# Optimization experiments

Measured on AMD Instinct MI355X. Metric: run time of the kernel, lower is better.

## Reference

```python
import jax, jax.numpy as jnp
import numpy as np

BN_EPS = 1e-5
TEMPERATURE = 256 ** 0.5  # sqrt(c2), since cv3 = ScaledDotProductAttention(c2)


def conv_bn_silu(x, w, gamma, beta, mean, var):
    # Conv2d(k=3, s=1, pad='same', bias=False) -> BatchNorm2d (running stats) -> SiLU
    y = jax.lax.conv_general_dilated(
        x, w, window_strides=(1, 1), padding='SAME',
        dimension_numbers=('NCHW', 'OIHW', 'NCHW'))
    scale = (gamma / jnp.sqrt(var + BN_EPS))[None, :, None, None]
    shift = (beta - mean * gamma / jnp.sqrt(var + BN_EPS))[None, :, None, None]
    y = y * scale + shift
    return y * jax.nn.sigmoid(y)  # SiLU


def setup_inputs() -> dict:
    key = jax.random.key(0)
    ks = jax.random.split(key, 8)
    B, C, H, W = 16, 256, 64, 64
    Ch = 128  # hidden channels c_ = int(c2 * e)
    x = jax.random.normal(ks[0], (B, C, H, W), dtype=jnp.float32)
    w1 = jax.random.normal(ks[1], (Ch, C, 3, 3), dtype=jnp.float32) * 0.05
    g1 = jnp.ones((Ch,), jnp.float32) + 0.1 * jax.random.normal(ks[2], (Ch,), dtype=jnp.float32)
    b1 = 0.1 * jax.random.normal(ks[3], (Ch,), dtype=jnp.float32)
    m1 = 0.1 * jax.random.normal(ks[4], (Ch,), dtype=jnp.float32)
    v1 = jnp.ones((Ch,), jnp.float32) + 0.5 * jax.random.uniform(ks[5], (Ch,), dtype=jnp.float32)
    w2 = jax.random.normal(ks[6], (C, Ch, 3, 3), dtype=jnp.float32) * 0.05
    g2 = jnp.ones((C,), jnp.float32)
    b2 = jnp.zeros((C,), jnp.float32)
    m2 = 0.1 * jax.random.normal(ks[7], (C,), dtype=jnp.float32)
    v2 = jnp.ones((C,), jnp.float32) + 0.5 * jax.random.uniform(jax.random.fold_in(key, 99), (C,), dtype=jnp.float32)
    return {"x": x, "w1": w1, "g1": g1, "b1": b1, "m1": m1, "v1": v1,
            "w2": w2, "g2": g2, "b2": b2, "m2": m2, "v2": v2}


def reference(x, w1, g1, b1, m1, v1, w2, g2, b2, m2, v2):
    y = conv_bn_silu(x, w1, g1, b1, m1, v1)       # [B, 128, H, W]
    y = conv_bn_silu(y, w2, g2, b2, m2, v2)       # [B, 256, H, W]
    B, C, H, W = y.shape
    q = y.reshape(B, C, H * W)                    # q = k^T = v, all views of y
    # channel-channel attention: scores [B, C, C]
    scores = jnp.einsum('bcn,bdn->bcd', q / TEMPERATURE, q)
    attn = jax.nn.softmax(scores, axis=-1)        # dropout is identity in eval
    out = jnp.einsum('bcd,bdn->bcn', attn, q).reshape(B, C, H, W)
    return x + out  # shortcut: c1 == c2
```

## Files before the change

### kernel.cpp

```cpp
#include <hip/hip_runtime.h>
#include <math.h>

#define BB 16
#define C1 256
#define CHD 128
#define NN 4096
#define INV_T (1.0f/16.0f)

typedef _Float16 half8 __attribute__((ext_vector_type(8)));
typedef __attribute__((ext_vector_type(4))) float f32x4;
typedef __attribute__((ext_vector_type(16))) float f32x16;

__device__ inline unsigned short f2h(float f) {
    _Float16 h = (_Float16)f;
    return __builtin_bit_cast(unsigned short, h);
}

#define GLDS(g, l) __builtin_amdgcn_global_load_lds(                              \
    (const __attribute__((address_space(1))) unsigned int*)(g),                   \
    (__attribute__((address_space(3))) unsigned int*)(l), 16, 0, 0)

__device__ inline void xcd_remap(int& bx, int& by, int& bz) {
    int gx = gridDim.x, gy = gridDim.y;
    int lin = blockIdx.x + gx * (blockIdx.y + gy * blockIdx.z);
    int cpx = (gx * gy * (int)gridDim.z) >> 3;
    lin = (lin & 7) * cpx + (lin >> 3);
    bx = lin % gx; int t = lin / gx; by = t % gy; bz = t / gy;
}

__global__ __launch_bounds__(256) void nchw_to_nhwc_f16(
    const float* __restrict__ x, unsigned short* __restrict__ xh, int C)
{
    const int c0 = blockIdx.x * 64;
    const int hp = blockIdx.y;
    const int b  = blockIdx.z;
    const int nCk = C >> 4;

    if (hp == 0 || hp == 65) {
        for (int idx = threadIdx.x; idx < 1024; idx += 256) {
            int w = idx >> 4, cq = (idx & 15) * 4;
            ushort4 z; z.x = z.y = z.z = z.w = 0;
            *(ushort4*)&xh[((((size_t)b * nCk + (c0 >> 4) + (cq >> 4)) * 66 + hp) * 64 + w) * 16
                           + (cq & 15)] = z;
        }
        return;
    }
    const int h = hp - 1;
    __shared__ float ts[64][65];
    for (int idx = threadIdx.x; idx < 4096; idx += 256) {
        int cl = idx >> 6, w = idx & 63;
        ts[cl][w] = x[(((size_t)b * C + c0 + cl) * 64 + h) * 64 + w];
    }
    __syncthreads();
    for (int idx = threadIdx.x; idx < 1024; idx += 256) {
        int w = idx >> 4, cq = (idx & 15) * 4;
        ushort4 o;
        o.x = f2h(ts[cq + 0][w]); o.y = f2h(ts[cq + 1][w]);
        o.z = f2h(ts[cq + 2][w]); o.w = f2h(ts[cq + 3][w]);
        *(ushort4*)&xh[((((size_t)b * nCk + (c0 >> 4) + (cq >> 4)) * 66 + hp) * 64 + w) * 16
                       + (cq & 15)] = o;
    }
}

__global__ __launch_bounds__(256) void pack_w_kernel(
    const float* __restrict__ w, unsigned short* __restrict__ wT, int Cout, int Cin)
{
    int idx = blockIdx.x * 256 + threadIdx.x;
    int total = Cout * Cin * 9;
    if (idx >= total) return;
    int ci = idx % Cin; int t = idx / Cin; int co = t % Cout; int kk = t / Cout;
    wT[((((size_t)(ci >> 4)) * 9 + kk) * Cout + co) * 16 + (ci & 15)] =
        f2h(w[((size_t)co * Cin + ci) * 9 + kk]);
}

__global__ __launch_bounds__(256) void zero_y1h_pads(unsigned short* __restrict__ y1h)
{
    int idx = blockIdx.x * 256 + threadIdx.x;
    int b   = idx >> 12;
    int ck  = (idx >> 9) & 7;
    int row = ((idx >> 8) & 1) ? 65 : 0;
    int w   = (idx >> 2) & 63;
    int qtr = idx & 3;
    ushort4 z; z.x = z.y = z.z = z.w = 0;
    *(ushort4*)&y1h[((((size_t)b * 8 + ck) * 66 + row) * 64 + w) * 16 + qtr * 4] = z;
}

__global__ __launch_bounds__(512, 4) void conv_mfma_kernel(
    const unsigned short* __restrict__ xh, const unsigned short* __restrict__ wT,
    const float* __restrict__ gamma, const float* __restrict__ beta,
    const float* __restrict__ mean, const float* __restrict__ var,
    unsigned short* __restrict__ outNHWC,
    unsigned short* __restrict__ yhi, unsigned short* __restrict__ yhiT,
    int Cin, int Cout)
{
    int bx, by, bz;
    xcd_remap(bx, by, bz);
    const int tid  = threadIdx.x;
    const int wid  = tid >> 6;
    const int lane = tid & 63;
    const int l31  = lane & 31;
    const int hi   = lane >> 5;
    const int coBase = bx * 64;
    const int h0     = by * 8;
    const int b      = bz;
    const int nCk    = Cin >> 4;

    __shared__ __align__(16) unsigned short smem[39552];
    __shared__ float bnsc[64], bnsh[64];

    if (tid < 64) {
        int co = coBase + tid;
        float sc = gamma[co] * rsqrtf(var[co] + 1e-5f);
        bnsc[tid] = sc;
        bnsh[tid] = beta[co] - mean[co] * sc;
    }
    if (tid < 160) {
        int cell = tid >> 2;
        int part = tid & 3;
        int buf  = cell & 1;
        int col  = ((cell >> 1) & 1) ? 65 : 0;
        int r    = cell >> 2;
        ushort4 z; z.x = z.y = z.z = z.w = 0;
        *(ushort4*)&smem[buf * 10560 + (r * 66 + col) * 16 + part * 4] = z;
    }

    auto stage = [&](int sel, int ck) {
        unsigned short* wsd = smem + 21120 + sel * 9216;
        unsigned short* xsd = smem + sel * 10560;
        for (int it = wid; it < 38; it += 8) {
            if (it < 18) {
                int kk = it >> 1, h = it & 1;
                const unsigned short* g =
                    wT + (((size_t)ck * 9 + kk) * Cout + coBase + h * 32) * 16 + lane * 8;
                GLDS(g, wsd + (kk * 64 + h * 32) * 16);
            } else {
                int j = it - 18;
                int r = j >> 1, hf = j & 1;
                const unsigned short* g =
                    xh + ((((size_t)b * nCk + ck) * 66 + h0 + r) * 64 + hf * 32) * 16 + lane * 8;
                GLDS(g, xsd + (r * 66 + 1 + hf * 32) * 16);
            }
        }
    };

    stage(0, 0);
    __syncthreads();

    f32x16 acc[2][2] = {};

    int sel = 0;
    for (int ck = 0; ck < nCk; ck++) {
        if (ck + 1 < nCk) stage(sel ^ 1, ck + 1);

        const unsigned short* wsb = smem + 21120 + sel * 9216;
        const unsigned short* xsb = smem + sel * 10560;
        __builtin_amdgcn_s_setprio(1);
#pragma unroll
        for (int kk = 0; kk < 9; kk++) {
            const int kh = kk / 3, kw = kk % 3;
            half8 a0 = *(const half8*)&wsb[(kk * 64 +      l31) * 16 + hi * 8];
            half8 a1 = *(const half8*)&wsb[(kk * 64 + 32 + l31) * 16 + hi * 8];
            const unsigned short* xr = &xsb[((wid + kh) * 66 + l31 + kw) * 16 + hi * 8];
            half8 b0 = *(const half8*)xr;
            half8 b1 = *(const half8*)&xr[32 * 16];
            acc[0][0] = __builtin_amdgcn_mfma_f32_32x32x16_f16(a0, b0, acc[0][0], 0, 0, 0);
            acc[0][1] = __builtin_amdgcn_mfma_f32_32x32x16_f16(a0, b1, acc[0][1], 0, 0, 0);
            acc[1][0] = __builtin_amdgcn_mfma_f32_32x32x16_f16(a1, b0, acc[1][0], 0, 0, 0);
            acc[1][1] = __builtin_amdgcn_mfma_f32_32x32x16_f16(a1, b1, acc[1][1], 0, 0, 0);
        }
        __builtin_amdgcn_s_setprio(0);
        __syncthreads();
        sel ^= 1;
    }

    const int orow = h0 + wid;
    const bool isConv1 = (outNHWC != nullptr);

    __syncthreads();

#pragma unroll
    for (int mi = 0; mi < 2; mi++)
#pragma unroll
        for (int ni = 0; ni < 2; ni++) {
            f32x16 a = acc[mi][ni];
            int w = ni * 32 + l31;
            int swz = ((l31 + wid) & 7) << 3;
#pragma unroll
            for (int rq = 0; rq < 4; rq++) {
                int c0 = mi * 32 + rq * 8 + hi * 4;
                ushort4 o; unsigned short* op = (unsigned short*)&o;
#pragma unroll
                for (int r = 0; r < 4; r++) {
                    float t = a[rq * 4 + r] * bnsc[c0 + r] + bnsh[c0 + r];
                    float s = t / (1.f + __expf(-t));
                    op[r] = f2h(s);
                    if (!isConv1)
                        yhi[(((size_t)b * Cout + coBase + c0 + r) * 64 + orow) * 64 + w] = op[r];
                }
                *(ushort4*)&smem[wid * 4096 + w * 64 + (c0 ^ swz)] = o;
            }
        }
    __syncthreads();

    const int ckB = bx * 4;
    const int nCkOut = Cout >> 4;
#pragma unroll
    for (int j = 0; j < 8; j++) {
        int g   = j * 512 + tid;
        int s   = g & 1;
        int w   = (g >> 1) & 63;
        int row = (g >> 7) & 7;
        int ck  = g >> 10;
        uint4 v = *(const uint4*)&smem[row * 4096 + w * 64 +
                     (((ck * 2 + s) * 8) ^ (((w + row) & 7) << 3))];
        if (isConv1) {
            *(uint4*)&outNHWC[((((size_t)b * nCkOut + ckB + ck) * 66 + h0 + row + 1) * 64 + w) * 16
                              + s * 8] = v;
        } else {
            *(uint4*)&yhiT[(((size_t)b * nCkOut + ckB + ck) * 4096 + (size_t)(h0 + row) * 64 + w) * 16
                           + s * 8] = v;
        }
    }
}

__global__ __launch_bounds__(256) void scores_mfma_kernel(
    const unsigned short* __restrict__ yhi, float* __restrict__ scores)
{
    static const int TI[10] = {0,0,0,0,1,1,1,2,2,3};
    static const int TJ[10] = {0,1,2,3,1,2,3,2,3,3};
    int bx, by, bz;
    xcd_remap(bx, by, bz);
    const int b  = bz;
    const int kh = by;
    const int ti = TI[bx], tj = TJ[bx];
    const int cB = ti * 64;
    const int dB = tj * 64;
    const int tid  = threadIdx.x;
    const int wid  = tid >> 6;
    const int lane = tid & 63;
    const int ln   = lane & 15;
    const int q    = lane >> 4;
    const int wm   = wid >> 1, wn = wid & 1;

    float* scp = scores + (size_t)kh * 1048576;

    __shared__ unsigned short As[64 * 128];
    __shared__ unsigned short Bs[64 * 128];

    const int rl = lane >> 4;
    const int gl = lane & 15;

    f32x4 acc[2][2] = {};

    for (int ck = kh * 16; ck < kh * 16 + 16; ck++) {
        const int n0 = ck * 128;
        for (int it = wid; it < 32; it += 4) {
            const int tile = it >> 4;
            const int j = it & 15;
            const int r = j * 4 + rl;
            const int gq = gl ^ (r & 7);
            const int rowAbs = (tile ? dB : cB) + r;
            const unsigned short* g =
                yhi + ((size_t)b * 256 + rowAbs) * 4096 + n0 + gq * 8;
            GLDS(g, (tile ? Bs : As) + j * 512);
        }
        __syncthreads();

#pragma unroll
        for (int kwin = 0; kwin < 4; kwin++) {
            half8 ah[2], bh[2];
#pragma unroll
            for (int mi = 0; mi < 2; mi++) {
                int row = wm * 32 + mi * 16 + ln;
                ah[mi] = *(const half8*)&As[row * 128 + ((kwin * 4 + q) ^ (ln & 7)) * 8];
            }
#pragma unroll
            for (int ni = 0; ni < 2; ni++) {
                int row = wn * 32 + ni * 16 + ln;
                bh[ni] = *(const half8*)&Bs[row * 128 + ((kwin * 4 + q) ^ (ln & 7)) * 8];
            }
#pragma unroll
            for (int mi = 0; mi < 2; mi++)
#pragma unroll
                for (int ni = 0; ni < 2; ni++)
                    acc[mi][ni] = __builtin_amdgcn_mfma_f32_16x16x32_f16(
                        ah[mi], bh[ni], acc[mi][ni], 0, 0, 0);
        }
        __syncthreads();
    }

#pragma unroll
    for (int mi = 0; mi < 2; mi++)
#pragma unroll
        for (int ni = 0; ni < 2; ni++) {
            f32x4 a = acc[mi][ni];
            float vals[4];
            vals[0] = a.x * INV_T; vals[1] = a.y * INV_T;
            vals[2] = a.z * INV_T; vals[3] = a.w * INV_T;
            int c0 = cB + wm * 32 + mi * 16 + q * 4;
            int d  = dB + wn * 32 + ni * 16 + ln;
#pragma unroll
            for (int r = 0; r < 4; r++)
                scp[((size_t)b * C1 + c0 + r) * C1 + d] = vals[r];
            if (ti != tj) {
                float4 tv = {vals[0], vals[1], vals[2], vals[3]};
                *(float4*)&scp[((size_t)b * C1 + d) * C1 + c0] = tv;
            }
        }
}

__global__ __launch_bounds__(64) void softmax_kernel(
    const float* __restrict__ scores, unsigned short* __restrict__ attn16)
{
    const int row = blockIdx.x;
    const float* p = scores + (size_t)row * C1;
    const int lane = threadIdx.x;

    float4 v0 = ((const float4*)p)[lane];
    float4 v1 = ((const float4*)(p + 1048576))[lane];
    float4 v;
    v.x = v0.x + v1.x; v.y = v0.y + v1.y;
    v.z = v0.z + v1.z; v.w = v0.w + v1.w;
    float m = fmaxf(fmaxf(v.x, v.y), fmaxf(v.z, v.w));
#pragma unroll
    for (int off = 32; off >= 1; off >>= 1)
        m = fmaxf(m, __shfl_xor(m, off, 64));

    float4 e;
    e.x = expf(v.x - m); e.y = expf(v.y - m);
    e.z = expf(v.z - m); e.w = expf(v.w - m);
    float s = e.x + e.y + e.z + e.w;
#pragma unroll
    for (int off = 32; off >= 1; off >>= 1)
        s += __shfl_xor(s, off, 64);
    float inv = 1.f / s;
    ushort4 o;
    o.x = f2h(e.x * inv); o.y = f2h(e.y * inv);
    o.z = f2h(e.z * inv); o.w = f2h(e.w * inv);
    *(ushort4*)&attn16[(size_t)row * C1 + lane * 4] = o;
}

__global__ __launch_bounds__(256) void out_mfma_kernel(
    const unsigned short* __restrict__ attn16, const unsigned short* __restrict__ yhiT,
    const float* __restrict__ x, float* __restrict__ out)
{
    int bx, by, bz;
    xcd_remap(bx, by, bz);
    const int b  = bz;
    const int cB = by * 64;
    const int nB = bx * 128;
    const int tid  = threadIdx.x;
    const int wid  = tid >> 6;
    const int lane = tid & 63;
    const int ln   = lane & 15;
    const int q    = lane >> 4;
    const int wm   = wid >> 1, wn = wid & 1;

    __shared__ unsigned short As[64 * 64];
    __shared__ unsigned short Bs[4 * 128 * 16];

    const int r8 = lane >> 3;
    const int gq = (lane & 7) ^ r8;

    f32x4 acc[2][4] = {};

    for (int ck = 0; ck < 4; ck++) {
        const int d0 = ck * 64;
        for (int it = wid; it < 24; it += 4) {
            if (it < 8) {
                const unsigned short* g =
                    attn16 + ((size_t)b * 256 + cB + it * 8 + r8) * 256 + d0 + gq * 8;
                GLDS(g, As + it * 512);
            } else {
                int j = it - 8;
                int u = j >> 2, part = j & 3;
                const unsigned short* g =
                    yhiT + (((size_t)b * 16 + ck * 4 + u) * 4096 + nB + part * 32) * 16 + lane * 8;
                GLDS(g, Bs + (u * 128 + part * 32) * 16);
            }
        }
        __syncthreads();

#pragma unroll
        for (int kwin = 0; kwin < 2; kwin++) {
            const int cc = (((kwin * 4 + q) ^ (ln & 7))) * 8;
            const int gK = kwin * 4 + q;
            half8 af[2], bfr[4];
#pragma unroll
            for (int mi = 0; mi < 2; mi++)
                af[mi] = *(const half8*)&As[(wm * 32 + mi * 16 + ln) * 64 + cc];
#pragma unroll
            for (int ni = 0; ni < 4; ni++) {
                int row = wn * 64 + ni * 16 + ln;
                bfr[ni] = *(const half8*)&Bs[(gK >> 1) * 2048 + row * 16 + (gK & 1) * 8];
            }
#pragma unroll
            for (int mi = 0; mi < 2; mi++)
#pragma unroll
                for (int ni = 0; ni < 4; ni++)
                    acc[mi][ni] = __builtin_amdgcn_mfma_f32_16x16x32_f16(
                        af[mi], bfr[ni], acc[mi][ni], 0, 0, 0);
        }
        __syncthreads();
    }

#pragma unroll
    for (int mi = 0; mi < 2; mi++)
#pragma unroll
        for (int ni = 0; ni < 4; ni++) {
            f32x4 a = acc[mi][ni];
            float vals[4] = {a.x, a.y, a.z, a.w};
#pragma unroll
            for (int r = 0; r < 4; r++) {
                int c = cB + wm * 32 + mi * 16 + q * 4 + r;
                int n = nB + wn * 64 + ni * 16 + ln;
                size_t o = ((size_t)b * C1 + c) * NN + n;
                out[o] = x[o] + vals[r];
            }
        }
}

extern "C" void kernel_launch(void* const* d_in, const int* in_sizes, int n_in,
                              void* d_out, int out_size, void* d_ws, size_t ws_size,
                              hipStream_t stream)
{
    const float* x  = (const float*)d_in[0];
    const float* w1 = (const float*)d_in[1];
    const float* g1 = (const float*)d_in[2];
    const float* b1 = (const float*)d_in[3];
    const float* m1 = (const float*)d_in[4];
    const float* v1 = (const float*)d_in[5];
    const float* w2 = (const float*)d_in[6];
    const float* g2 = (const float*)d_in[7];
    const float* b2 = (const float*)d_in[8];
    const float* m2 = (const float*)d_in[9];
    const float* v2 = (const float*)d_in[10];
    float* out = (float*)d_out;

    unsigned short* xh   = (unsigned short*)d_ws;
    unsigned short* y1h  = xh  + (size_t)17301504;
    unsigned short* wt1  = y1h + (size_t)8650752;
    unsigned short* wt2  = wt1 + (size_t)294912;
    unsigned short* yhiT = wt2 + (size_t)294912;
    unsigned short* yhi  = xh;
    float*          sc   = (float*)y1h;
    unsigned short* attn16 = (unsigned short*)(sc + 2097152);

    nchw_to_nhwc_f16<<<dim3(C1 / 64, 66, BB), 256, 0, stream>>>(x, xh, C1);
    pack_w_kernel<<<(9 * CHD * C1 + 255) / 256, 256, 0, stream>>>(w1, wt1, CHD, C1);
    pack_w_kernel<<<(9 * C1 * CHD + 255) / 256, 256, 0, stream>>>(w2, wt2, C1, CHD);
    zero_y1h_pads<<<256, 256, 0, stream>>>(y1h);

    conv_mfma_kernel<<<dim3(CHD / 64, 8, BB), 512, 0, stream>>>(
        xh, wt1, g1, b1, m1, v1, y1h, nullptr, nullptr, C1, CHD);
    conv_mfma_kernel<<<dim3(C1 / 64, 8, BB), 512, 0, stream>>>(
        y1h, wt2, g2, b2, m2, v2, nullptr, yhi, yhiT, CHD, C1);

    scores_mfma_kernel<<<dim3(10, 2, BB), 256, 0, stream>>>(yhi, sc);
    softmax_kernel<<<dim3(BB * C1), 64, 0, stream>>>(sc, attn16);
    out_mfma_kernel<<<dim3(NN / 128, 4, BB), 256, 0, stream>>>(attn16, yhiT, x, out);
}
```

Baseline: 299.8 us.

## Split 16-channel chunks into two 8-channel halves for conv LDS layout

Changes the packed fp16 layout of inputs, weights and the conv1 intermediate from [..][w][16 channels] to [..][half][w][8 channels], so each MFMA operand read in the conv kernel hits contiguous 16-byte rows per half-wave. The goal is to remove LDS bank conflicts caused by the 32-byte stride between lanes in the old interleaved layout. Producers, padding zeroing, staging and the conv1 output store are all updated to match. The risk is a layout mismatch between producers and consumers, or different conflict patterns at the padded column offsets.

```diff
diff --git a/kernel.cpp b/kernel.cpp
--- a/kernel.cpp
+++ b/kernel.cpp
@@ -39,9 +39,10 @@
     if (hp == 0 || hp == 65) {
         for (int idx = threadIdx.x; idx < 1024; idx += 256) {
             int w = idx >> 4, cq = (idx & 15) * 4;
+            int ck = (c0 >> 4) + (cq >> 4), half = (cq >> 3) & 1, rem = cq & 7;
             ushort4 z; z.x = z.y = z.z = z.w = 0;
-            *(ushort4*)&xh[((((size_t)b * nCk + (c0 >> 4) + (cq >> 4)) * 66 + hp) * 64 + w) * 16
-                           + (cq & 15)] = z;
+            *(ushort4*)&xh[(((((size_t)b * nCk + ck) * 66 + hp) * 2 + half) * 64 + w) * 8
+                           + rem] = z;
         }
         return;
     }
@@ -54,11 +55,12 @@
     __syncthreads();
     for (int idx = threadIdx.x; idx < 1024; idx += 256) {
         int w = idx >> 4, cq = (idx & 15) * 4;
+        int ck = (c0 >> 4) + (cq >> 4), half = (cq >> 3) & 1, rem = cq & 7;
         ushort4 o;
         o.x = f2h(ts[cq + 0][w]); o.y = f2h(ts[cq + 1][w]);
         o.z = f2h(ts[cq + 2][w]); o.w = f2h(ts[cq + 3][w]);
-        *(ushort4*)&xh[((((size_t)b * nCk + (c0 >> 4) + (cq >> 4)) * 66 + hp) * 64 + w) * 16
-                       + (cq & 15)] = o;
+        *(ushort4*)&xh[(((((size_t)b * nCk + ck) * 66 + hp) * 2 + half) * 64 + w) * 8
+                       + rem] = o;
     }
 }
 
@@ -69,7 +71,8 @@
     int total = Cout * Cin * 9;
     if (idx >= total) return;
     int ci = idx % Cin; int t = idx / Cin; int co = t % Cout; int kk = t / Cout;
-    wT[((((size_t)(ci >> 4)) * 9 + kk) * Cout + co) * 16 + (ci & 15)] =
+    int ck = ci >> 4, half = (ci >> 3) & 1, rem = ci & 7;
+    wT[((((size_t)ck * 9 + kk) * 2 + half) * Cout + co) * 8 + rem] =
         f2h(w[((size_t)co * Cin + ci) * 9 + kk]);
 }
 
@@ -79,10 +82,9 @@
     int b   = idx >> 12;
     int ck  = (idx >> 9) & 7;
     int row = ((idx >> 8) & 1) ? 65 : 0;
-    int w   = (idx >> 2) & 63;
-    int qtr = idx & 3;
+    int inner = (idx & 255) * 4;
     ushort4 z; z.x = z.y = z.z = z.w = 0;
-    *(ushort4*)&y1h[((((size_t)b * 8 + ck) * 66 + row) * 64 + w) * 16 + qtr * 4] = z;
+    *(ushort4*)&y1h[(((size_t)b * 8 + ck) * 66 + row) * 1024 + inner] = z;
 }
 
 __global__ __launch_bounds__(512, 4) void conv_mfma_kernel(
@@ -114,14 +116,14 @@
         bnsc[tid] = sc;
         bnsh[tid] = beta[co] - mean[co] * sc;
     }
-    if (tid < 160) {
-        int cell = tid >> 2;
-        int part = tid & 3;
-        int buf  = cell & 1;
-        int col  = ((cell >> 1) & 1) ? 65 : 0;
-        int r    = cell >> 2;
+    if (tid < 80) {
+        int buf  = tid & 1;
+        int col  = ((tid >> 1) & 1) ? 65 : 0;
+        int half = (tid >> 2) & 1;
+        int r    = tid >> 3;
         ushort4 z; z.x = z.y = z.z = z.w = 0;
-        *(ushort4*)&smem[buf * 10560 + (r * 66 + col) * 16 + part * 4] = z;
+        *(ushort4*)&smem[buf * 10560 + ((r * 2 + half) * 66 + col) * 8] = z;
+        *(ushort4*)&smem[buf * 10560 + ((r * 2 + half) * 66 + col) * 8 + 4] = z;
     }
 
     auto stage = [&](int sel, int ck) {
@@ -129,16 +131,16 @@
         unsigned short* xsd = smem + sel * 10560;
         for (int it = wid; it < 38; it += 8) {
             if (it < 18) {
-                int kk = it >> 1, h = it & 1;
+                int kk = it >> 1, half = it & 1;
                 const unsigned short* g =
-                    wT + (((size_t)ck * 9 + kk) * Cout + coBase + h * 32) * 16 + lane * 8;
-                GLDS(g, wsd + (kk * 64 + h * 32) * 16);
+                    wT + ((((size_t)ck * 9 + kk) * 2 + half) * Cout + coBase) * 8 + lane * 8;
+                GLDS(g, wsd + (kk * 2 + half) * 512);
             } else {
                 int j = it - 18;
-                int r = j >> 1, hf = j & 1;
+                int r = j >> 1, half = j & 1;
                 const unsigned short* g =
-                    xh + ((((size_t)b * nCk + ck) * 66 + h0 + r) * 64 + hf * 32) * 16 + lane * 8;
-                GLDS(g, xsd + (r * 66 + 1 + hf * 32) * 16);
+                    xh + ((((size_t)b * nCk + ck) * 66 + h0 + r) * 2 + half) * 512 + lane * 8;
+                GLDS(g, xsd + ((r * 2 + half) * 66 + 1) * 8);
             }
         }
     };
@@ -158,11 +160,12 @@
 #pragma unroll
         for (int kk = 0; kk < 9; kk++) {
             const int kh = kk / 3, kw = kk % 3;
-            half8 a0 = *(const half8*)&wsb[(kk * 64 +      l31) * 16 + hi * 8];
-            half8 a1 = *(const half8*)&wsb[(kk * 64 + 32 + l31) * 16 + hi * 8];
-            const unsigned short* xr = &xsb[((wid + kh) * 66 + l31 + kw) * 16 + hi * 8];
+            half8 a0 = *(const half8*)&wsb[((kk * 2 + hi) * 64 +      l31) * 8];
+            half8 a1 = *(const half8*)&wsb[((kk * 2 + hi) * 64 + 32 + l31) * 8];
+            const unsigned short* xr =
+                &xsb[(((wid + kh) * 2 + hi) * 66 + l31 + kw) * 8];
             half8 b0 = *(const half8*)xr;
-            half8 b1 = *(const half8*)&xr[32 * 16];
+            half8 b1 = *(const half8*)&xr[32 * 8];
             acc[0][0] = __builtin_amdgcn_mfma_f32_32x32x16_f16(a0, b0, acc[0][0], 0, 0, 0);
             acc[0][1] = __builtin_amdgcn_mfma_f32_32x32x16_f16(a0, b1, acc[0][1], 0, 0, 0);
             acc[1][0] = __builtin_amdgcn_mfma_f32_32x32x16_f16(a1, b0, acc[1][0], 0, 0, 0);
@@ -214,8 +217,8 @@
         uint4 v = *(const uint4*)&smem[row * 4096 + w * 64 +
                      (((ck * 2 + s) * 8) ^ (((w + row) & 7) << 3))];
         if (isConv1) {
-            *(uint4*)&outNHWC[((((size_t)b * nCkOut + ckB + ck) * 66 + h0 + row + 1) * 64 + w) * 16
-                              + s * 8] = v;
+            *(uint4*)&outNHWC[((((((size_t)b * nCkOut + ckB + ck) * 66 + h0 + row + 1) * 2 + s)
+                               * 64 + w) * 8)] = v;
         } else {
             *(uint4*)&yhiT[(((size_t)b * nCkOut + ckB + ck) * 4096 + (size_t)(h0 + row) * 64 + w) * 16
                            + s * 8] = v;
```

After: 307.5 us. 2.5% more time.
